# Kernel tuning notes

Hardware: AMD Instinct MI355X
Metric: run time of the kernel (lower is better)

Reference implementation:

```python
import jax, jax.numpy as jnp
import numpy as np

N = 262144   # cohort size (k_n)
M = 8192     # number of ordinal anchor indices (len(Hj))


def setup_inputs() -> dict:
    key = jax.random.key(0)
    k1, k2, k3, k4, k5 = jax.random.split(key, 5)
    time = jax.random.uniform(k1, (N,), dtype=jnp.float32) * 1000.0
    event = (jax.random.uniform(k2, (N,), dtype=jnp.float32) < 0.3).astype(jnp.float32)
    y_true0 = jnp.stack([time, event], axis=1)          # [N,2] (time, event)
    y_true1 = y_true0                                    # second head labels (unused by loss)
    y_pred0 = jax.random.normal(k3, (N, 1), dtype=jnp.float32) * 0.1  # xbeta head 0
    y_pred1 = jax.random.normal(k4, (N, 1), dtype=jnp.float32) * 0.1  # xbeta head 1
    Hj = jnp.sort(jax.random.randint(k5, (M,), 0, N, dtype=jnp.int32))  # static event indices into sorted order
    log_vars = jnp.zeros((2, 1), dtype=jnp.float32)      # layer weights log_var0, log_var1
    return {"y_true0": y_true0, "y_true1": y_true1, "y_pred0": y_pred0,
            "y_pred1": y_pred1, "Hj": Hj, "log_vars": log_vars}


def reference(y_true0, y_true1, y_pred0, y_pred1, Hj, log_vars):
    n = y_true0.shape[0]
    # top_k with k = n == full descending sort by time
    _, order = jax.lax.top_k(y_true0[:, 0], n)

    # ---- neg_log_pl (Cox negative partial log-likelihood, per-sample vector) ----
    xbeta = y_pred0[order, 0]                 # [N] sorted by descending time
    event = y_true0[order, 1]                 # [N]
    denom = jnp.cumsum(jnp.exp(xbeta))        # risk-set cumulative sum
    lossA = -(event * (xbeta - jnp.log(denom)))  # [N]

    # ---- ordinal_loss0 (pairwise ranking over event indices Hj in sorted order) ----
    # intended math: for each j, for ii >= j: cost += 1 - exp(xbeta[Hj[j]] - xbeta[Hj[ii]])
    xb = y_pred1[order, 0]                    # [N] sorted
    xh = xb[Hj]                               # [M]
    m = Hj.shape[0]
    rec = 1.0 - jnp.exp(xh[:, None] - xh[None, :])   # [M,M] rec[j,ii]
    mask = jnp.triu(jnp.ones((m, m), dtype=bool))    # ii >= j
    cost2 = jnp.sum(jnp.where(mask, rec, 0.0))

    # ---- multi_loss combination with learned log variances ----
    lv0 = log_vars[0, 0]
    lv1 = log_vars[1, 0]
    precision1 = jnp.clip(jnp.exp(-lv1), 0.0, 1.0)
    loss = jnp.sum(lossA + lv0) + (precision1 * cost2 + lv1)
    return loss


if __name__ == "__main__":
    out = reference(**setup_inputs())
    print(out)
```

## Files before the change

### kernel.cpp

```cpp
#include <hip/hip_runtime.h>
#include <math.h>


#define BSHIFT 12
#define NBUCK (1 << 19)
#define SCAN_BLK 1024
#define NPART (NBUCK / SCAN_BLK)
#define RMAX 4

__global__ void k_hist(const float2* __restrict__ yt0, const float* __restrict__ yp0,
                       int n, int rmask,
                       unsigned* __restrict__ count, float* __restrict__ expsum,
                       unsigned* __restrict__ seq) {
  int i = blockIdx.x * blockDim.x + threadIdx.x;
  if (i >= n) return;
  int r = blockIdx.x & rmask;
  unsigned key = __float_as_uint(yt0[i].x);
  unsigned b = key >> BSHIFT;
  seq[i] = atomicAdd(&count[(size_t)r * NBUCK + b], 1u);
  atomicAdd(&expsum[(size_t)r * NBUCK + b], expf(yp0[i]));
}

__global__ void k_scan_reduce(const unsigned* __restrict__ count, const float* __restrict__ expsum,
                              int nrep,
                              unsigned* __restrict__ countTot, float* __restrict__ expTot,
                              unsigned* __restrict__ offArr,
                              unsigned* __restrict__ cntPart, float* __restrict__ expPart) {
  __shared__ unsigned sc[SCAN_BLK];
  __shared__ float sf[SCAN_BLK];
  int t = threadIdx.x, g = blockIdx.x;
  int b = NBUCK - 1 - (g * SCAN_BLK + t);
  unsigned tot = 0;
  float ftot = 0.f;
  for (int r = 0; r < nrep; ++r) {
    offArr[(size_t)r * NBUCK + b] = tot;
    tot += count[(size_t)r * NBUCK + b];
    ftot += expsum[(size_t)r * NBUCK + b];
  }
  countTot[b] = tot;
  expTot[b] = ftot;
  sc[t] = tot;
  sf[t] = ftot;
  __syncthreads();
  for (int s = SCAN_BLK / 2; s > 0; s >>= 1) {
    if (t < s) { sc[t] += sc[t + s]; sf[t] += sf[t + s]; }
    __syncthreads();
  }
  if (t == 0) { cntPart[g] = sc[0]; expPart[g] = sf[0]; }
}

__global__ void k_scan_final(const unsigned* __restrict__ count, const float* __restrict__ expsum,
                             const unsigned* __restrict__ cntPart, const float* __restrict__ expPart,
                             unsigned* __restrict__ sfxCnt, float* __restrict__ sfxExp) {
  __shared__ unsigned sc[SCAN_BLK];
  __shared__ float sf[SCAN_BLK];
  int t = threadIdx.x, g = blockIdx.x;
  sc[t] = (t < g) ? cntPart[t] : 0u;
  sf[t] = (t < g) ? expPart[t] : 0.f;
  __syncthreads();
  for (int s = SCAN_BLK / 2; s > 0; s >>= 1) {
    if (t < s) { sc[t] += sc[t + s]; sf[t] += sf[t + s]; }
    __syncthreads();
  }
  unsigned basC = sc[0];
  float basF = sf[0];
  __syncthreads();
  int b = NBUCK - 1 - (g * SCAN_BLK + t);
  sc[t] = count[b];
  sf[t] = expsum[b];
  __syncthreads();
  for (int off = 1; off < SCAN_BLK; off <<= 1) {
    unsigned c = 0; float f = 0.f;
    if (t >= off) { c = sc[t - off]; f = sf[t - off]; }
    __syncthreads();
    sc[t] += c; sf[t] += f;
    __syncthreads();
  }
  sfxCnt[b] = sc[t] + basC;
  sfxExp[b] = sf[t] + basF;
}

__global__ void k_scatter(const float2* __restrict__ yt0, const float* __restrict__ yp0, int n,
                          int rmask,
                          const unsigned* __restrict__ countTot, const unsigned* __restrict__ sfxCnt,
                          const unsigned* __restrict__ offArr, const unsigned* __restrict__ seq,
                          uint2* __restrict__ skey2, unsigned* __restrict__ sidx) {
  int i = blockIdx.x * blockDim.x + threadIdx.x;
  if (i >= n) return;
  int r = blockIdx.x & rmask;
  float2 te = yt0[i];
  unsigned key = __float_as_uint(te.x);
  unsigned ev = (te.y != 0.f) ? 0x80000000u : 0u;
  unsigned b = key >> BSHIFT;
  unsigned start = sfxCnt[b] - countTot[b];
  unsigned pos = start + offArr[(size_t)r * NBUCK + b] + seq[i];
  uint2 v; v.x = key; v.y = __float_as_uint(expf(yp0[i]));
  skey2[pos] = v;
  sidx[pos] = (unsigned)i | ev;
}

__global__ void k_main(const float* __restrict__ yp1, const int* __restrict__ Hj,
                       int n, int m,
                       const unsigned* __restrict__ countTot, const float* __restrict__ expTot,
                       const unsigned* __restrict__ sfxCnt, const float* __restrict__ sfxExp,
                       const uint2* __restrict__ skey2, const unsigned* __restrict__ sidx,
                       float* __restrict__ xh, double* __restrict__ accum) {
  int p = blockIdx.x * blockDim.x + threadIdx.x;
  double contrib = 0.0;
  if (p < n) {
    uint2 kv = skey2[p];
    unsigned key = kv.x;
    float e = __uint_as_float(kv.y);
    unsigned sidv = sidx[p];
    unsigned idx = sidv & 0x7FFFFFFFu;
    bool ev = (sidv >> 31) != 0u;
    unsigned b = key >> BSHIFT;
    unsigned end = sfxCnt[b];
    unsigned start = end - countTot[b];
    if (end > (unsigned)n) end = (unsigned)n;
    if (start > end) start = end;
    float wsum = 0.f;
    unsigned wcnt = 0;
    unsigned q = start;
    while (q + 8 <= end) {
      uint2 v[8];
      #pragma unroll
      for (int k = 0; k < 8; ++k) v[k] = skey2[q + k];
      #pragma unroll
      for (int k = 0; k < 8; ++k) {
        if (v[k].x > key) { wsum += __uint_as_float(v[k].y); wcnt++; }
        else if (v[k].x == key && (sidx[q + k] & 0x7FFFFFFFu) < idx) {
          wsum += __uint_as_float(v[k].y); wcnt++;
        }
      }
      q += 8;
    }
    for (; q < end; ++q) {
      uint2 v = skey2[q];
      if (v.x > key) { wsum += __uint_as_float(v.y); wcnt++; }
      else if (v.x == key && (sidx[q] & 0x7FFFFFFFu) < idx) {
        wsum += __uint_as_float(v.y); wcnt++;
      }
    }
    float denom = (sfxExp[b] - expTot[b]) + wsum + e;
    int rank = (int)(start + wcnt);
    contrib = ev ? (double)logf(denom / e) : 0.0;
    int lo = 0, hi = m;
    while (lo < hi) { int mid = (lo + hi) >> 1; if (Hj[mid] < rank) lo = mid + 1; else hi = mid; }
    if (lo < m && Hj[lo] == rank) {
      float xb1 = yp1[idx];
      for (int j = lo; j < m && Hj[j] == rank; ++j) xh[j] = xb1;
    }
  }
  __shared__ double red[256];
  int t = threadIdx.x;
  red[t] = contrib;
  __syncthreads();
  for (int s = 128; s > 0; s >>= 1) {
    if (t < s) red[t] += red[t + s];
    __syncthreads();
  }
  if (t == 0) atomicAdd(accum, red[0]);
}

__global__ void k_final(const float* __restrict__ xh, int m,
                        const double* __restrict__ accum, const float* __restrict__ log_vars,
                        int n, float* __restrict__ out) {
  __shared__ float wtots[16];
  __shared__ double dred[1024];
  int t = threadIdx.x;
  int lane = t & 63;
  int w = t >> 6;
  double acc = 0.0;
  float carry = 0.f;
  int passes = (m + 8191) / 8192;
  for (int pss = passes - 1; pss >= 0; --pss) {
    int base = pss * 8192 + t * 8;
    float x[8], eb[8];
    float c = 0.f;
    #pragma unroll
    for (int k = 0; k < 8; ++k) {
      int j = base + k;
      x[k] = (j < m) ? xh[j] : 0.f;
      eb[k] = (j < m) ? expf(-x[k]) : 0.f;
      c += eb[k];
    }
    float s = c;
    #pragma unroll
    for (int d = 1; d < 64; d <<= 1) {
      float o = __shfl_down(s, d, 64);
      if (lane + d < 64) s += o;
    }
    float wtot = __shfl(s, 0, 64);
    if (lane == 0) wtots[w] = wtot;
    __syncthreads();
    float after = 0.f;
    #pragma unroll
    for (int w2 = 0; w2 < 16; ++w2) if (w2 > w) after += wtots[w2];
    float ptot = 0.f;
    #pragma unroll
    for (int w2 = 0; w2 < 16; ++w2) ptot += wtots[w2];
    float S = (s - c) + after + carry;
    #pragma unroll
    for (int k = 7; k >= 0; --k) {
      int j = base + k;
      S += eb[k];
      if (j < m) acc += (double)(expf(x[k]) * S);
    }
    __syncthreads();
    carry += ptot;
  }
  dred[t] = acc;
  __syncthreads();
  for (int s2 = 512; s2 > 0; s2 >>= 1) {
    if (t < s2) dred[t] += dred[t + s2];
    __syncthreads();
  }
  if (t == 0) {
    double T = (double)m * (double)(m + 1) * 0.5;
    double cost2 = T - dred[0];
    float lv0 = log_vars[0], lv1 = log_vars[1];
    float prec1 = fminf(expf(-lv1), 1.0f);
    double loss = *accum + (double)n * (double)lv0 + (double)prec1 * cost2 + (double)lv1;
    out[0] = (float)loss;
  }
}

extern "C" void kernel_launch(void* const* d_in, const int* in_sizes, int n_in,
                              void* d_out, int out_size, void* d_ws, size_t ws_size,
                              hipStream_t stream) {
  const float2* yt0 = (const float2*)d_in[0];
  const float*  yp0 = (const float*)d_in[2];
  const float*  yp1 = (const float*)d_in[3];
  const int*    Hj  = (const int*)d_in[4];
  const float*  lv  = (const float*)d_in[5];
  int n = in_sizes[0] / 2;
  int m = in_sizes[4];

  int nrep = RMAX;
  {
    size_t need = (size_t)nrep * NBUCK * 4 * 3
                + (size_t)NBUCK * 4 * 4
                + (size_t)NPART * 4 * 2
                + (size_t)n * 4 * 4
                + (size_t)m * 4 + 256;
    if (ws_size < need) nrep = 1;
  }
  int rmask = nrep - 1;

  char* ws = (char*)d_ws;
  size_t off = 0;
  unsigned* count  = (unsigned*)(ws + off); off += (size_t)nrep * NBUCK * 4;
  float*    expsum = (float*)(ws + off);    off += (size_t)nrep * NBUCK * 4;
  double*   accum  = (double*)(ws + off);   off += 16;
  size_t zbytes = off;
  unsigned* offArr  = (unsigned*)(ws + off); off += (size_t)nrep * NBUCK * 4;
  unsigned* countTot= (unsigned*)(ws + off); off += (size_t)NBUCK * 4;
  float*    expTot  = (float*)(ws + off);    off += (size_t)NBUCK * 4;
  unsigned* cntPart = (unsigned*)(ws + off); off += (size_t)NPART * 4;
  float*    expPart = (float*)(ws + off);    off += (size_t)NPART * 4;
  unsigned* sfxCnt  = (unsigned*)(ws + off); off += (size_t)NBUCK * 4;
  float*    sfxExp  = (float*)(ws + off);    off += (size_t)NBUCK * 4;
  unsigned* seq     = (unsigned*)(ws + off); off += (size_t)n * 4;
  uint2*    skey2   = (uint2*)(ws + off);    off += (size_t)n * 8;
  unsigned* sidx    = (unsigned*)(ws + off); off += (size_t)n * 4;
  float*    xh      = (float*)(ws + off);    off += (size_t)m * 4;

  hipMemsetAsync(d_ws, 0, zbytes, stream);

  int blk = 256;
  int g_n = (n + blk - 1) / blk;
  k_hist<<<g_n, blk, 0, stream>>>(yt0, yp0, n, rmask, count, expsum, seq);
  k_scan_reduce<<<NPART, SCAN_BLK, 0, stream>>>(count, expsum, nrep,
                                                countTot, expTot, offArr, cntPart, expPart);
  k_scan_final<<<NPART, SCAN_BLK, 0, stream>>>(countTot, expTot, cntPart, expPart, sfxCnt, sfxExp);
  k_scatter<<<g_n, blk, 0, stream>>>(yt0, yp0, n, rmask, countTot, sfxCnt, offArr, seq,
                                     skey2, sidx);
  k_main<<<g_n, blk, 0, stream>>>(yp1, Hj, n, m, countTot, expTot, sfxCnt, sfxExp,
                                  skey2, sidx, xh, accum);
  k_final<<<1, 1024, 0, stream>>>(xh, m, accum, lv, n, (float*)d_out);
}
```

Measured before the change: 154.2 us.

## Replace per-bucket exp-sum atomics and scans with a prefix scan over sorted exps

Drops the float atomicAdd of exp values per bucket in the histogram kernel, along with the float channels of both bucket scan kernels. The bucket-level suffix exp sum is now computed by a block-wise inclusive prefix scan over the sorted exp values. k_main combines a shared-memory scan of the block totals with a preS lookup to get the cross-bucket risk sum. This removes float atomics on 2M bucket slots and halves the scan traffic, at the cost of an extra kernel launch and a redundant 256-entry scan in every k_main block. It also assumes seParts is at most 256.

```diff
diff --git a/kernel.cpp b/kernel.cpp
--- a/kernel.cpp
+++ b/kernel.cpp
@@ -7,77 +7,64 @@
 #define SCAN_BLK 1024
 #define NPART (NBUCK / SCAN_BLK)
 #define RMAX 4
-
-__global__ void k_hist(const float2* __restrict__ yt0, const float* __restrict__ yp0,
-                       int n, int rmask,
-                       unsigned* __restrict__ count, float* __restrict__ expsum,
-                       unsigned* __restrict__ seq) {
+#define SEBLK 1024
+
+__global__ void k_hist(const float2* __restrict__ yt0, int n, int rmask,
+                       unsigned* __restrict__ count, unsigned* __restrict__ seq) {
   int i = blockIdx.x * blockDim.x + threadIdx.x;
   if (i >= n) return;
   int r = blockIdx.x & rmask;
   unsigned key = __float_as_uint(yt0[i].x);
   unsigned b = key >> BSHIFT;
   seq[i] = atomicAdd(&count[(size_t)r * NBUCK + b], 1u);
-  atomicAdd(&expsum[(size_t)r * NBUCK + b], expf(yp0[i]));
-}
-
-__global__ void k_scan_reduce(const unsigned* __restrict__ count, const float* __restrict__ expsum,
-                              int nrep,
-                              unsigned* __restrict__ countTot, float* __restrict__ expTot,
+}
+
+__global__ void k_scan_reduce(const unsigned* __restrict__ count, int nrep,
+                              unsigned* __restrict__ countTot,
                               unsigned* __restrict__ offArr,
-                              unsigned* __restrict__ cntPart, float* __restrict__ expPart) {
+                              unsigned* __restrict__ cntPart) {
   __shared__ unsigned sc[SCAN_BLK];
-  __shared__ float sf[SCAN_BLK];
   int t = threadIdx.x, g = blockIdx.x;
   int b = NBUCK - 1 - (g * SCAN_BLK + t);
   unsigned tot = 0;
-  float ftot = 0.f;
   for (int r = 0; r < nrep; ++r) {
     offArr[(size_t)r * NBUCK + b] = tot;
     tot += count[(size_t)r * NBUCK + b];
-    ftot += expsum[(size_t)r * NBUCK + b];
   }
   countTot[b] = tot;
-  expTot[b] = ftot;
   sc[t] = tot;
-  sf[t] = ftot;
   __syncthreads();
   for (int s = SCAN_BLK / 2; s > 0; s >>= 1) {
-    if (t < s) { sc[t] += sc[t + s]; sf[t] += sf[t + s]; }
-    __syncthreads();
-  }
-  if (t == 0) { cntPart[g] = sc[0]; expPart[g] = sf[0]; }
-}
-
-__global__ void k_scan_final(const unsigned* __restrict__ count, const float* __restrict__ expsum,
-                             const unsigned* __restrict__ cntPart, const float* __restrict__ expPart,
-                             unsigned* __restrict__ sfxCnt, float* __restrict__ sfxExp) {
+    if (t < s) sc[t] += sc[t + s];
+    __syncthreads();
+  }
+  if (t == 0) cntPart[g] = sc[0];
+}
+
+__global__ void k_scan_final(const unsigned* __restrict__ count,
+                             const unsigned* __restrict__ cntPart,
+                             unsigned* __restrict__ sfxCnt) {
   __shared__ unsigned sc[SCAN_BLK];
-  __shared__ float sf[SCAN_BLK];
   int t = threadIdx.x, g = blockIdx.x;
   sc[t] = (t < g) ? cntPart[t] : 0u;
-  sf[t] = (t < g) ? expPart[t] : 0.f;
   __syncthreads();
   for (int s = SCAN_BLK / 2; s > 0; s >>= 1) {
-    if (t < s) { sc[t] += sc[t + s]; sf[t] += sf[t + s]; }
+    if (t < s) sc[t] += sc[t + s];
     __syncthreads();
   }
   unsigned basC = sc[0];
-  float basF = sf[0];
   __syncthreads();
   int b = NBUCK - 1 - (g * SCAN_BLK + t);
   sc[t] = count[b];
-  sf[t] = expsum[b];
   __syncthreads();
   for (int off = 1; off < SCAN_BLK; off <<= 1) {
-    unsigned c = 0; float f = 0.f;
-    if (t >= off) { c = sc[t - off]; f = sf[t - off]; }
-    __syncthreads();
-    sc[t] += c; sf[t] += f;
+    unsigned c = 0;
+    if (t >= off) c = sc[t - off];
+    __syncthreads();
+    sc[t] += c;
     __syncthreads();
   }
   sfxCnt[b] = sc[t] + basC;
-  sfxExp[b] = sf[t] + basF;
 }
 
 __global__ void k_scatter(const float2* __restrict__ yt0, const float* __restrict__ yp0, int n,
@@ -99,13 +86,46 @@
   sidx[pos] = (unsigned)i | ev;
 }
 
+__global__ void k_scan_se(const uint2* __restrict__ skey2, int n,
+                          float* __restrict__ preS, float* __restrict__ blockTot) {
+  __shared__ float sf[SEBLK];
+  int t = threadIdx.x;
+  int p = blockIdx.x * SEBLK + t;
+  float v = (p < n) ? __uint_as_float(skey2[p].y) : 0.f;
+  sf[t] = v;
+  __syncthreads();
+  for (int off = 1; off < SEBLK; off <<= 1) {
+    float a = 0.f;
+    if (t >= off) a = sf[t - off];
+    __syncthreads();
+    sf[t] += a;
+    __syncthreads();
+  }
+  if (p < n) preS[p] = sf[t];
+  if (t == SEBLK - 1) blockTot[blockIdx.x] = sf[t];
+}
+
 __global__ void k_main(const float* __restrict__ yp1, const int* __restrict__ Hj,
-                       int n, int m,
-                       const unsigned* __restrict__ countTot, const float* __restrict__ expTot,
-                       const unsigned* __restrict__ sfxCnt, const float* __restrict__ sfxExp,
+                       int n, int m, int seParts,
+                       const unsigned* __restrict__ countTot,
+                       const unsigned* __restrict__ sfxCnt,
                        const uint2* __restrict__ skey2, const unsigned* __restrict__ sidx,
+                       const float* __restrict__ preS, const float* __restrict__ blockTot,
                        float* __restrict__ xh, double* __restrict__ accum) {
-  int p = blockIdx.x * blockDim.x + threadIdx.x;
+  __shared__ float pb[256];
+  __shared__ double red[256];
+  int t = threadIdx.x;
+  pb[t] = (t < seParts) ? blockTot[t] : 0.f;
+  __syncthreads();
+  for (int off = 1; off < 256; off <<= 1) {
+    float a = 0.f;
+    if (t >= off) a = pb[t - off];
+    __syncthreads();
+    pb[t] += a;
+    __syncthreads();
+  }
+
+  int p = blockIdx.x * blockDim.x + t;
   double contrib = 0.0;
   if (p < n) {
     uint2 kv = skey2[p];
@@ -142,7 +162,10 @@
         wsum += __uint_as_float(v.y); wcnt++;
       }
     }
-    float denom = (sfxExp[b] - expTot[b]) + wsum + e;
+    unsigned sb = start >> 10;
+    float cross = ((sb > 0) ? pb[sb - 1] : 0.f)
+                + ((start & 1023u) ? preS[start - 1] : 0.f);
+    float denom = cross + wsum + e;
     int rank = (int)(start + wcnt);
     contrib = ev ? (double)logf(denom / e) : 0.0;
     int lo = 0, hi = m;
@@ -152,8 +175,6 @@
       for (int j = lo; j < m && Hj[j] == rank; ++j) xh[j] = xb1;
     }
   }
-  __shared__ double red[256];
-  int t = threadIdx.x;
   red[t] = contrib;
   __syncthreads();
   for (int s = 128; s > 0; s >>= 1) {
@@ -236,13 +257,15 @@
   const float*  lv  = (const float*)d_in[5];
   int n = in_sizes[0] / 2;
   int m = in_sizes[4];
+  int seParts = (n + SEBLK - 1) / SEBLK;
 
   int nrep = RMAX;
   {
-    size_t need = (size_t)nrep * NBUCK * 4 * 3
-                + (size_t)NBUCK * 4 * 4
-                + (size_t)NPART * 4 * 2
-                + (size_t)n * 4 * 4
+    size_t need = (size_t)nrep * NBUCK * 4 * 2
+                + (size_t)NBUCK * 4 * 2
+                + (size_t)NPART * 4
+                + (size_t)n * 4 * 5
+                + 1024 * 4
                 + (size_t)m * 4 + 256;
     if (ws_size < need) nrep = 1;
   }
@@ -251,32 +274,30 @@
   char* ws = (char*)d_ws;
   size_t off = 0;
   unsigned* count  = (unsigned*)(ws + off); off += (size_t)nrep * NBUCK * 4;
-  float*    expsum = (float*)(ws + off);    off += (size_t)nrep * NBUCK * 4;
   double*   accum  = (double*)(ws + off);   off += 16;
   size_t zbytes = off;
   unsigned* offArr  = (unsigned*)(ws + off); off += (size_t)nrep * NBUCK * 4;
   unsigned* countTot= (unsigned*)(ws + off); off += (size_t)NBUCK * 4;
-  float*    expTot  = (float*)(ws + off);    off += (size_t)NBUCK * 4;
   unsigned* cntPart = (unsigned*)(ws + off); off += (size_t)NPART * 4;
-  float*    expPart = (float*)(ws + off);    off += (size_t)NPART * 4;
   unsigned* sfxCnt  = (unsigned*)(ws + off); off += (size_t)NBUCK * 4;
-  float*    sfxExp  = (float*)(ws + off);    off += (size_t)NBUCK * 4;
   unsigned* seq     = (unsigned*)(ws + off); off += (size_t)n * 4;
   uint2*    skey2   = (uint2*)(ws + off);    off += (size_t)n * 8;
   unsigned* sidx    = (unsigned*)(ws + off); off += (size_t)n * 4;
+  float*    preS    = (float*)(ws + off);    off += (size_t)n * 4;
+  float*    blockTot= (float*)(ws + off);    off += 1024 * 4;
   float*    xh      = (float*)(ws + off);    off += (size_t)m * 4;
 
   hipMemsetAsync(d_ws, 0, zbytes, stream);
 
   int blk = 256;
   int g_n = (n + blk - 1) / blk;
-  k_hist<<<g_n, blk, 0, stream>>>(yt0, yp0, n, rmask, count, expsum, seq);
-  k_scan_reduce<<<NPART, SCAN_BLK, 0, stream>>>(count, expsum, nrep,
-                                                countTot, expTot, offArr, cntPart, expPart);
-  k_scan_final<<<NPART, SCAN_BLK, 0, stream>>>(countTot, expTot, cntPart, expPart, sfxCnt, sfxExp);
+  k_hist<<<g_n, blk, 0, stream>>>(yt0, n, rmask, count, seq);
+  k_scan_reduce<<<NPART, SCAN_BLK, 0, stream>>>(count, nrep, countTot, offArr, cntPart);
+  k_scan_final<<<NPART, SCAN_BLK, 0, stream>>>(countTot, cntPart, sfxCnt);
   k_scatter<<<g_n, blk, 0, stream>>>(yt0, yp0, n, rmask, countTot, sfxCnt, offArr, seq,
                                      skey2, sidx);
-  k_main<<<g_n, blk, 0, stream>>>(yp1, Hj, n, m, countTot, expTot, sfxCnt, sfxExp,
-                                  skey2, sidx, xh, accum);
+  k_scan_se<<<seParts, SEBLK, 0, stream>>>(skey2, n, preS, blockTot);
+  k_main<<<g_n, blk, 0, stream>>>(yp1, Hj, n, m, seParts, countTot, sfxCnt,
+                                  skey2, sidx, preS, blockTot, xh, accum);
   k_final<<<1, 1024, 0, stream>>>(xh, m, accum, lv, n, (float*)d_out);
 }
```

New measurement: 139.5 us. 1.11x faster.
